# Optimization experiments

Hardware: AMD Instinct MI355X
Metric: run time of the kernel (lower is better)

The kernel has to match this reference:

```python
import jax, jax.numpy as jnp
import numpy as np

DIM = 384
HD = 64
SCALE = float(HD ** 0.5)


def _linear_params(key, out_f, in_f):
    kw, kb = jax.random.split(key)
    bound = 1.0 / np.sqrt(in_f)
    W = jax.random.uniform(kw, (out_f, in_f), jnp.float32, -bound, bound)
    b = jax.random.uniform(kb, (out_f,), jnp.float32, -bound, bound)
    return W, b


def setup_inputs() -> dict:
    key = jax.random.key(0)
    ks = jax.random.split(key, 12)
    N = 8192
    situation = jax.random.normal(ks[0], (DIM,), jnp.float32)
    turn_embeddings = jax.random.normal(ks[1], (N, DIM), jnp.float32)
    bilinear_scores = jax.random.normal(ks[2], (N,), jnp.float32)
    Wt, bt = _linear_params(ks[3], HD, DIM + 1)      # turn_proj
    Ws, bs = _linear_params(ks[4], HD, DIM)          # situation_proj
    Wsaq, bsaq = _linear_params(ks[5], HD, HD)
    Wsak, bsak = _linear_params(ks[6], HD, HD)
    Wsav, bsav = _linear_params(ks[7], HD, HD)
    Wcq, bcq = _linear_params(ks[8], HD, HD)
    Wck, bck = _linear_params(ks[9], HD, HD)
    Wcv, bcv = _linear_params(ks[10], HD, HD)
    # score_head is zero-initialized in the module; use small random values so
    # the output is non-trivial for kernel correctness testing.
    Wsc, bsc = _linear_params(ks[11], 1, HD)
    residual_gate = jnp.float32(-5.0)
    return dict(situation=situation, turn_embeddings=turn_embeddings,
                bilinear_scores=bilinear_scores,
                Wt=Wt, bt=bt, Ws=Ws, bs=bs,
                Wsaq=Wsaq, bsaq=bsaq, Wsak=Wsak, bsak=bsak, Wsav=Wsav, bsav=bsav,
                Wcq=Wcq, bcq=bcq, Wck=Wck, bck=bck, Wcv=Wcv, bcv=bcv,
                Wsc=Wsc, bsc=bsc, residual_gate=residual_gate)


def reference(situation, turn_embeddings, bilinear_scores,
              Wt, bt, Ws, bs,
              Wsaq, bsaq, Wsak, bsak, Wsav, bsav,
              Wcq, bcq, Wck, bck, Wcv, bcv,
              Wsc, bsc, residual_gate):
    # [N, dim+1] = [turn_embedding; bilinear_score]
    turn_features = jnp.concatenate([turn_embeddings, bilinear_scores[:, None]], axis=-1)
    turn_hidden = turn_features @ Wt.T + bt                      # [N, HD]
    # self-attention among turns (dropout = identity, eval mode)
    sa_q = turn_hidden @ Wsaq.T + bsaq
    sa_k = turn_hidden @ Wsak.T + bsak
    sa_v = turn_hidden @ Wsav.T + bsav
    sa_weights = jax.nn.softmax((sa_q @ sa_k.T) / SCALE, axis=-1)  # [N, N]
    turn_hidden = turn_hidden + sa_weights @ sa_v
    # sigmoid cross-attention against the single situation vector
    sit_hidden = (situation @ Ws.T + bs)[None, :]                # [1, HD]
    ca_q = turn_hidden @ Wcq.T + bcq                             # [N, HD]
    ca_k = sit_hidden @ Wck.T + bck                              # [1, HD]
    ca_v = sit_hidden @ Wcv.T + bcv                              # [1, HD]
    ca_weights = jax.nn.sigmoid((ca_q @ ca_k.T) / SCALE)         # [N, 1]
    combined = turn_hidden + ca_weights * ca_v                   # [N, HD]
    attention_scores = (combined @ Wsc.T + bsc)[:, 0]            # [N]
    gate = jax.nn.sigmoid(residual_gate)
    return (1.0 - gate) * bilinear_scores + gate * attention_scores
```

## Files before the change

kernel.cpp:

```cpp
#include <hip/hip_runtime.h>
#include <hip/hip_bf16.h>

typedef __attribute__((ext_vector_type(8))) short short8;
typedef __attribute__((ext_vector_type(4))) float f32x4;
typedef __attribute__((ext_vector_type(2))) long long2t;

__device__ __forceinline__ short f2bf(float x) {
  union { float f; unsigned u; } a; a.f = x;
  unsigned r = (a.u + 0x7FFFu + ((a.u >> 16) & 1u)) >> 16;
  return (short)r;
}
__device__ __forceinline__ float bf2f(short x) {
  union { unsigned u; float f; } a; a.u = ((unsigned)(unsigned short)x) << 16;
  return a.f;
}
__device__ __forceinline__ unsigned cvtpk(float lo, float hi) {
  unsigned r;
  asm("v_cvt_pk_bf16_f32 %0, %1, %2" : "=v"(r) : "v"(lo), "v"(hi));
  return r;
}
__device__ __forceinline__ unsigned pk8(float a, float b, float c, float d) {
  unsigned lo, hi;
  asm("v_cvt_pk_fp8_f32 %0, %1, %2" : "=v"(lo) : "v"(a), "v"(b));
  asm("v_cvt_pk_fp8_f32 %0, %1, %2" : "=v"(hi) : "v"(c), "v"(d));
  return (lo & 0xffffu) | (hi << 16);
}
__device__ __forceinline__ long2t as_l2(uint4 v) {
  union { uint4 u; long2t l; } cc; cc.u = v; return cc.l;
}
__device__ __forceinline__ void gload16(const void* g, void* l) {
  __builtin_amdgcn_global_load_lds((const __attribute__((address_space(1))) unsigned int*)g,
                                   (__attribute__((address_space(3))) unsigned int*)l, 16, 0, 0);
}

__global__ __launch_bounds__(256) void ca_proj4(
    const float* __restrict__ te, const float* __restrict__ bil,
    const float* __restrict__ Wt, const float* __restrict__ bt,
    const float* __restrict__ Wsaq, const float* __restrict__ bq,
    const float* __restrict__ Wsak, const float* __restrict__ bk2,
    const float* __restrict__ Wsav, const float* __restrict__ bv,
    short* __restrict__ hb, unsigned char* __restrict__ qb8,
    unsigned char* __restrict__ kb8, unsigned char* __restrict__ vl8,
    const float* __restrict__ sit, const float* __restrict__ Ws, const float* __restrict__ bs,
    const float* __restrict__ Wck, const float* __restrict__ bck,
    const float* __restrict__ Wcv, const float* __restrict__ bcv,
    const float* __restrict__ Wcq, const float* __restrict__ bcq,
    const float* __restrict__ Wsc, float* __restrict__ u_ws, float* __restrict__ scal,
    int N) {
  __shared__ float Pp[8192];
  __shared__ short Hl[32][72];
  __shared__ unsigned char Q8[32][72];
  __shared__ unsigned char K8[32][72];
  __shared__ unsigned char V8s[64][32];
  __shared__ float part[4][64];
  __shared__ float sh[64], ck[64], cv[64];
  const int t = threadIdx.x;
  if ((int)blockIdx.x == (N >> 5)) {
    int j = t & 63, p = t >> 6;
    float a = 0.f;
    for (int d = p * 96; d < p * 96 + 96; ++d) a += Ws[j * 384 + d] * sit[d];
    part[p][j] = a;
    __syncthreads();
    if (t < 64) sh[t] = part[0][t] + part[1][t] + part[2][t] + part[3][t] + bs[t];
    __syncthreads();
    if (t < 64) {
      float kk = bck[t], vv = bcv[t];
      for (int d = 0; d < 64; ++d) { kk += Wck[t * 64 + d] * sh[d]; vv += Wcv[t * 64 + d] * sh[d]; }
      ck[t] = kk; cv[t] = vv;
    }
    __syncthreads();
    if (t < 64) {
      float uu = 0.f;
      for (int jj = 0; jj < 64; ++jj) uu += Wcq[jj * 64 + t] * ck[jj];
      u_ws[t] = uu;
    }
    if (t == 0) {
      float c0 = 0.f, cw = 0.f;
      for (int jj = 0; jj < 64; ++jj) { c0 += bcq[jj] * ck[jj]; cw += cv[jj] * Wsc[jj]; }
      scal[0] = c0; scal[1] = cw;
    }
    return;
  }
  const int lane = t & 63, w = t >> 6;
  const int g = lane >> 4, li = lane & 15;
  const int i0 = blockIdx.x * 32;

  f32x4 acc[2][4];
#pragma unroll
  for (int qs = 0; qs < 2; ++qs)
#pragma unroll
    for (int n = 0; n < 4; ++n) acc[qs][n] = (f32x4){0.f, 0.f, 0.f, 0.f};
  const int kw = w * 96;
#pragma unroll
  for (int ks = 0; ks < 3; ++ks) {
    short8 af[2];
#pragma unroll
    for (int qs = 0; qs < 2; ++qs) {
      const float* ap = te + (size_t)(i0 + qs * 16 + li) * 384 + kw + ks * 32 + g * 8;
      float4 a0 = *(const float4*)ap;
      float4 a1 = *(const float4*)(ap + 4);
      af[qs][0] = f2bf(a0.x); af[qs][1] = f2bf(a0.y); af[qs][2] = f2bf(a0.z); af[qs][3] = f2bf(a0.w);
      af[qs][4] = f2bf(a1.x); af[qs][5] = f2bf(a1.y); af[qs][6] = f2bf(a1.z); af[qs][7] = f2bf(a1.w);
    }
#pragma unroll
    for (int n = 0; n < 4; ++n) {
      short8 bf;
      const float* wp = Wt + (size_t)(n * 16 + li) * 385 + kw + ks * 32 + g * 8;
#pragma unroll
      for (int jj = 0; jj < 8; ++jj) bf[jj] = f2bf(wp[jj]);
      acc[0][n] = __builtin_amdgcn_mfma_f32_16x16x32_bf16(af[0], bf, acc[0][n], 0, 0, 0);
      acc[1][n] = __builtin_amdgcn_mfma_f32_16x16x32_bf16(af[1], bf, acc[1][n], 0, 0, 0);
    }
  }
#pragma unroll
  for (int qs = 0; qs < 2; ++qs)
#pragma unroll
    for (int n = 0; n < 4; ++n)
      *(f32x4*)&Pp[((w * 8 + qs * 4 + n) * 64 + lane) * 4] = acc[qs][n];
  __syncthreads();
#pragma unroll
  for (int ss = 0; ss < 2; ++ss) {
    int s = t + ss * 256;
    int qs2 = s >> 8, n2 = (s >> 6) & 3, lane2 = s & 63;
    int g2 = lane2 >> 4, li2 = lane2 & 15;
    int base = (qs2 * 4 + n2) * 256 + lane2 * 4;
    f32x4 v0 = *(const f32x4*)&Pp[base];
    f32x4 v1 = *(const f32x4*)&Pp[base + 2048];
    f32x4 v2 = *(const f32x4*)&Pp[base + 4096];
    f32x4 v3 = *(const f32x4*)&Pp[base + 6144];
    int col = n2 * 16 + li2;
    float wc = Wt[(size_t)col * 385 + 384], bb = bt[col];
#pragma unroll
    for (int r = 0; r < 4; ++r) {
      int row = qs2 * 16 + g2 * 4 + r;
      float val = v0[r] + v1[r] + v2[r] + v3[r] + bb + bil[i0 + row] * wc;
      Hl[row][col] = f2bf(val);
    }
  }
  __syncthreads();
  {
    int row = t >> 3, seg = t & 7;
    *(uint4*)&hb[(size_t)(i0 + row) * 64 + seg * 8] = *(uint4*)&Hl[row][seg * 8];
  }
  short8 ha[2][2];
#pragma unroll
  for (int qs = 0; qs < 2; ++qs)
#pragma unroll
    for (int ks = 0; ks < 2; ++ks)
      ha[qs][ks] = *(const short8*)&Hl[qs * 16 + li][ks * 32 + g * 8];
  const float* Wm[3] = {Wsaq, Wsak, Wsav};
  f32x4 pacc[3][2];
#pragma unroll
  for (int m = 0; m < 3; ++m)
#pragma unroll
    for (int qs = 0; qs < 2; ++qs) pacc[m][qs] = (f32x4){0.f, 0.f, 0.f, 0.f};
#pragma unroll
  for (int m = 0; m < 3; ++m)
#pragma unroll
    for (int ks = 0; ks < 2; ++ks) {
      const float* wp = Wm[m] + (size_t)(w * 16 + li) * 64 + ks * 32 + g * 8;
      float4 b0 = *(const float4*)wp;
      float4 b1 = *(const float4*)(wp + 4);
      short8 bf;
      bf[0] = f2bf(b0.x); bf[1] = f2bf(b0.y); bf[2] = f2bf(b0.z); bf[3] = f2bf(b0.w);
      bf[4] = f2bf(b1.x); bf[5] = f2bf(b1.y); bf[6] = f2bf(b1.z); bf[7] = f2bf(b1.w);
      pacc[m][0] = __builtin_amdgcn_mfma_f32_16x16x32_bf16(ha[0][ks], bf, pacc[m][0], 0, 0, 0);
      pacc[m][1] = __builtin_amdgcn_mfma_f32_16x16x32_bf16(ha[1][ks], bf, pacc[m][1], 0, 0, 0);
    }
  const int col = w * 16 + li;
  const float QSC = 0.18033688011112042f;
  {
    float bbq = bq[col], bbk = bk2[col], bbv = bv[col];
#pragma unroll
    for (int qs = 0; qs < 2; ++qs) {
      unsigned uq = pk8((pacc[0][qs][0] + bbq) * QSC, (pacc[0][qs][1] + bbq) * QSC,
                        (pacc[0][qs][2] + bbq) * QSC, (pacc[0][qs][3] + bbq) * QSC);
      unsigned uk = pk8(pacc[1][qs][0] + bbk, pacc[1][qs][1] + bbk,
                        pacc[1][qs][2] + bbk, pacc[1][qs][3] + bbk);
      unsigned uv = pk8(pacc[2][qs][0] + bbv, pacc[2][qs][1] + bbv,
                        pacc[2][qs][2] + bbv, pacc[2][qs][3] + bbv);
#pragma unroll
      for (int r = 0; r < 4; ++r) {
        Q8[qs * 16 + g * 4 + r][col] = (unsigned char)(uq >> (8 * r));
        K8[qs * 16 + g * 4 + r][col] = (unsigned char)(uk >> (8 * r));
      }
      *(unsigned*)&V8s[col][qs * 16 + g * 4] = uv;
    }
  }
  __syncthreads();
  {
    const int h = t & 1, l2 = (t >> 1) & 63, loc = t >> 7;
    const int srow = (l2 & 15) + 16 * loc;
    const int scol = h * 32 + (l2 >> 4) * 8;
    unsigned long vq = *(const unsigned long*)&Q8[srow][scol];
    *(unsigned long*)(qb8 + ((size_t)((i0 >> 4) + loc) * 1024 + l2 * 16 + h * 8)) = vq;
    unsigned long vk = *(const unsigned long*)&K8[srow][scol];
    *(unsigned long*)(kb8 + ((size_t)((i0 >> 6) * 4 + ((i0 >> 4) & 3) + loc) * 1024 + l2 * 16 + h * 8)) = vk;
    const int dt = t >> 6, l3 = t & 63;
    unsigned long vv = *(const unsigned long*)&V8s[dt * 16 + (l3 & 15)][(l3 >> 4) * 8];
    *(unsigned long*)(vl8 + ((size_t)((i0 >> 6) * 4 + dt) * 1024 + l3 * 16 + ((i0 >> 5) & 1) * 8)) = vv;
  }
}

__global__ __launch_bounds__(128, 2) void ca_attn7(
    const uint4* __restrict__ qb8, const unsigned* __restrict__ kb8,
    const unsigned* __restrict__ vl8,
    unsigned* __restrict__ pOu, float* __restrict__ pL, int N) {
  __shared__ unsigned Kl[2][1024];
  __shared__ unsigned Vl[2][1024];
  __shared__ unsigned Pl[2][2][256];
  const int t = threadIdx.x, lane = t & 63, wid = t >> 6;
  const int g = lane >> 4, li = lane & 15;
  const int bid = blockIdx.x;
  const int sp = bid & 7, qblk = bid >> 3;
  const int i0 = qblk * 64 + wid * 32;
  const int ntil = N >> 9;
  const int tile0 = sp * ntil;

#define STG(b, T)                                                                                  \
  do {                                                                                             \
    gload16(kb8 + (((size_t)(T) * 4 + 2 * wid) << 8) + lane * 4,     &Kl[b][(2 * wid) * 256]);     \
    gload16(kb8 + (((size_t)(T) * 4 + 2 * wid + 1) << 8) + lane * 4, &Kl[b][(2 * wid + 1) * 256]); \
    gload16(vl8 + (((size_t)(T) * 4 + 2 * wid) << 8) + lane * 4,     &Vl[b][(2 * wid) * 256]);     \
    gload16(vl8 + (((size_t)(T) * 4 + 2 * wid + 1) << 8) + lane * 4, &Vl[b][(2 * wid + 1) * 256]); \
  } while (0)

  long2t qf[2];
  qf[0] = as_l2(qb8[(size_t)((i0 >> 4) + 0) * 64 + lane]);
  qf[1] = as_l2(qb8[(size_t)((i0 >> 4) + 1) * 64 + lane]);

  f32x4 acc[2][4];
  float rs[2] = {0.f, 0.f};
#pragma unroll
  for (int qs = 0; qs < 2; ++qs)
#pragma unroll
    for (int n = 0; n < 4; ++n) acc[qs][n] = (f32x4){0.f, 0.f, 0.f, 0.f};

  STG(0, tile0);
  asm volatile("s_waitcnt vmcnt(0)" ::: "memory");

  for (int tt = 0; tt < ntil; ++tt) {
    const int cur = tt & 1;
    __builtin_amdgcn_s_barrier();
    if (tt + 1 < ntil) STG(cur ^ 1, tile0 + tt + 1);

    f32x4 s4[2][4];
#pragma unroll
    for (int qs = 0; qs < 2; ++qs)
#pragma unroll
      for (int t4 = 0; t4 < 4; ++t4) s4[qs][t4] = (f32x4){0.f, 0.f, 0.f, 0.f};
    __builtin_amdgcn_s_setprio(1);
#pragma unroll
    for (int t4 = 0; t4 < 4; ++t4) {
      long2t kl = as_l2(*(const uint4*)&Kl[cur][t4 * 256 + lane * 4]);
      s4[0][t4] = __builtin_amdgcn_mfma_f32_16x16x32_fp8_fp8(kl.x, qf[0].x, s4[0][t4], 0, 0, 0);
      s4[0][t4] = __builtin_amdgcn_mfma_f32_16x16x32_fp8_fp8(kl.y, qf[0].y, s4[0][t4], 0, 0, 0);
      s4[1][t4] = __builtin_amdgcn_mfma_f32_16x16x32_fp8_fp8(kl.x, qf[1].x, s4[1][t4], 0, 0, 0);
      s4[1][t4] = __builtin_amdgcn_mfma_f32_16x16x32_fp8_fp8(kl.y, qf[1].y, s4[1][t4], 0, 0, 0);
    }
    __builtin_amdgcn_s_setprio(0);
#pragma unroll
    for (int qs = 0; qs < 2; ++qs) {
#pragma unroll
      for (int t4 = 0; t4 < 4; ++t4) {
        float p0, p1, p2, p3;
        asm("v_exp_f32 %0, %1" : "=v"(p0) : "v"(s4[qs][t4][0]));
        asm("v_exp_f32 %0, %1" : "=v"(p1) : "v"(s4[qs][t4][1]));
        asm("v_exp_f32 %0, %1" : "=v"(p2) : "v"(s4[qs][t4][2]));
        asm("v_exp_f32 %0, %1" : "=v"(p3) : "v"(s4[qs][t4][3]));
        rs[qs] += (p0 + p1) + (p2 + p3);
        unsigned u = pk8(p0, p1, p2, p3);
        Pl[wid][qs][(li + 16 * ((t4 & 1) * 2 + (g >> 1))) * 4 + (t4 >> 1) * 2 + (g & 1)] = u;
      }
    }
    asm volatile("s_waitcnt lgkmcnt(0)" ::: "memory");
    long2t pf0 = as_l2(*(const uint4*)&Pl[wid][0][lane * 4]);
    long2t pf1 = as_l2(*(const uint4*)&Pl[wid][1][lane * 4]);
    __builtin_amdgcn_s_setprio(1);
#pragma unroll
    for (int dt = 0; dt < 4; ++dt) {
      long2t vf = as_l2(*(const uint4*)&Vl[cur][dt * 256 + lane * 4]);
      acc[0][dt] = __builtin_amdgcn_mfma_f32_16x16x32_fp8_fp8(pf0.x, vf.x, acc[0][dt], 0, 0, 0);
      acc[0][dt] = __builtin_amdgcn_mfma_f32_16x16x32_fp8_fp8(pf0.y, vf.y, acc[0][dt], 0, 0, 0);
      acc[1][dt] = __builtin_amdgcn_mfma_f32_16x16x32_fp8_fp8(pf1.x, vf.x, acc[1][dt], 0, 0, 0);
      acc[1][dt] = __builtin_amdgcn_mfma_f32_16x16x32_fp8_fp8(pf1.y, vf.y, acc[1][dt], 0, 0, 0);
    }
    __builtin_amdgcn_s_setprio(0);
    asm volatile("s_waitcnt vmcnt(0)" ::: "memory");
  }
#undef STG

  const size_t ob = ((size_t)sp * (N >> 5) + (i0 >> 5)) * 2;
#pragma unroll
  for (int qs = 0; qs < 2; ++qs) {
#pragma unroll
    for (int dt = 0; dt < 4; ++dt) {
      uint2 wv;
      wv.x = cvtpk(acc[qs][dt][0], acc[qs][dt][1]);
      wv.y = cvtpk(acc[qs][dt][2], acc[qs][dt][3]);
      *(uint2*)&pOu[((ob + qs) * 4 + dt) * 128 + lane * 2] = wv;
    }
    float r2 = rs[qs] + __shfl_xor(rs[qs], 16, 64);
    r2 += __shfl_xor(r2, 32, 64);
    if (lane < 16) pL[(size_t)sp * N + i0 + qs * 16 + lane] = r2;
  }
}

__global__ __launch_bounds__(256) void ca_merge3(
    const short* __restrict__ hb, const unsigned* __restrict__ pOu, const float* __restrict__ pL,
    const float* __restrict__ u_ws, const float* __restrict__ scal,
    const float* __restrict__ bil, const float* __restrict__ Wsc,
    const float* __restrict__ bsc_p, const float* __restrict__ rgate_p,
    float* __restrict__ out, int N) {
  const int t = threadIdx.x;
  const int rp = t >> 3, e = t & 7;
  const int dt2 = e >> 1, li0 = (e & 1) * 8;
  const float gate = 1.f / (1.f + __expf(-rgate_p[0]));
  const float bsc = bsc_p[0], sc0 = scal[0], sc1 = scal[1];
  const int R0 = blockIdx.x * 64 + rp * 2;
  const int b32 = R0 >> 5, qs2 = (R0 >> 4) & 1, g2 = (R0 >> 2) & 3;
  const int rpair = (R0 & 3) >> 1;
  float o0[8], o1[8], L0 = 0.f, L1 = 0.f;
#pragma unroll
  for (int j = 0; j < 8; ++j) { o0[j] = 0.f; o1[j] = 0.f; }
#pragma unroll
  for (int sp2 = 0; sp2 < 8; ++sp2) {
    size_t base = ((((size_t)sp2 * (N >> 5) + b32) * 2 + qs2) * 4 + dt2) * 128
                  + (g2 * 16 + li0) * 2 + rpair;
#pragma unroll
    for (int j = 0; j < 8; ++j) {
      unsigned u = pOu[base + 2 * j];
      o0[j] += bf2f((short)(u & 0xffff));
      o1[j] += bf2f((short)(u >> 16));
    }
    L0 += pL[(size_t)sp2 * N + R0];
    L1 += pL[(size_t)sp2 * N + R0 + 1];
  }
  const float iL0 = 1.f / L0, iL1 = 1.f / L1;
  const int c0 = dt2 * 16 + li0;
  short8 hv0 = *(const short8*)&hb[(size_t)R0 * 64 + c0];
  short8 hv1 = *(const short8*)&hb[(size_t)(R0 + 1) * 64 + c0];
  float s1a = 0.f, s2a = 0.f, s1b = 0.f, s2b = 0.f;
#pragma unroll
  for (int j = 0; j < 8; ++j) {
    float uwsj = u_ws[c0 + j], wscj = Wsc[c0 + j];
    float h0 = bf2f(hv0[j]) + o0[j] * iL0;
    float h1 = bf2f(hv1[j]) + o1[j] * iL1;
    s1a += h0 * uwsj; s2a += h0 * wscj;
    s1b += h1 * uwsj; s2b += h1 * wscj;
  }
#pragma unroll
  for (int mask = 1; mask < 8; mask <<= 1) {
    s1a += __shfl_xor(s1a, mask, 64);
    s2a += __shfl_xor(s2a, mask, 64);
    s1b += __shfl_xor(s1b, mask, 64);
    s2b += __shfl_xor(s2b, mask, 64);
  }
  if (e == 0) {
    float cawa = 1.f / (1.f + __expf(-(s1a + sc0) * 0.125f));
    float cawb = 1.f / (1.f + __expf(-(s1b + sc0) * 0.125f));
    float scoreA = s2a + cawa * sc1 + bsc;
    float scoreB = s2b + cawb * sc1 + bsc;
    out[R0] = (1.f - gate) * bil[R0] + gate * scoreA;
    out[R0 + 1] = (1.f - gate) * bil[R0 + 1] + gate * scoreB;
  }
}

extern "C" void kernel_launch(void* const* d_in, const int* in_sizes, int n_in,
                              void* d_out, int out_size, void* d_ws, size_t ws_size,
                              hipStream_t stream) {
  const float* sit  = (const float*)d_in[0];
  const float* te   = (const float*)d_in[1];
  const float* bil  = (const float*)d_in[2];
  const float* Wt   = (const float*)d_in[3];
  const float* bt   = (const float*)d_in[4];
  const float* Ws   = (const float*)d_in[5];
  const float* bs   = (const float*)d_in[6];
  const float* Wsaq = (const float*)d_in[7];
  const float* bsaq = (const float*)d_in[8];
  const float* Wsak = (const float*)d_in[9];
  const float* bsak = (const float*)d_in[10];
  const float* Wsav = (const float*)d_in[11];
  const float* bsav = (const float*)d_in[12];
  const float* Wcq  = (const float*)d_in[13];
  const float* bcq  = (const float*)d_in[14];
  const float* Wck  = (const float*)d_in[15];
  const float* bck  = (const float*)d_in[16];
  const float* Wcv  = (const float*)d_in[17];
  const float* bcv  = (const float*)d_in[18];
  const float* Wsc  = (const float*)d_in[19];
  const float* bsc  = (const float*)d_in[20];
  const float* rgate= (const float*)d_in[21];
  const int N = in_sizes[2];

  char* w = (char*)d_ws;
  size_t off = 0;
  short* hbuf        = (short*)(w + off);         off += (size_t)N * 64 * 2;
  unsigned char* qb8 = (unsigned char*)(w + off); off += (size_t)N * 64;
  unsigned char* kb8 = (unsigned char*)(w + off); off += (size_t)N * 64;
  unsigned char* vl8 = (unsigned char*)(w + off); off += (size_t)N * 64;
  float* u_ws        = (float*)(w + off);         off += 64 * 4;
  float* scal        = (float*)(w + off);         off += 4 * 4;
  unsigned* pOu      = (unsigned*)(w + off);      off += (size_t)8 * N * 64 * 2;
  float* pL          = (float*)(w + off);         off += (size_t)8 * N * 4;

  ca_proj4<<<N / 32 + 1, 256, 0, stream>>>(te, bil, Wt, bt, Wsaq, bsaq, Wsak, bsak,
                                           Wsav, bsav, hbuf, qb8, kb8, vl8,
                                           sit, Ws, bs, Wck, bck, Wcv, bcv, Wcq, bcq, Wsc,
                                           u_ws, scal, N);
  ca_attn7<<<N / 8, 128, 0, stream>>>((const uint4*)qb8, (const unsigned*)kb8,
                                      (const unsigned*)vl8, pOu, pL, N);
  ca_merge3<<<N / 64, 256, 0, stream>>>(hbuf, pOu, pL, u_ws, scal, bil, Wsc, bsc, rgate,
                                        (float*)d_out, N);
}
```

Measured before the change: 50.56 us.

## Split turn projection by output columns per wave, drop split-K LDS reduction

The first projection GEMM changes from a split-K layout (each wave covering a quarter of K for all 64 output columns, then reducing partial sums through a 32KB shared buffer) to an output-column split where each wave owns 16 columns across the full K. This removes the partial-sum LDS buffer, one barrier and the reduction pass, and lowers LDS use, which may allow more blocks per CU. In exchange every wave now reads the whole 32x384 activation tile from global memory, four times the previous per-wave A traffic, and runs a longer serial chain of dependent MFMAs.

```diff
diff --git a/kernel.cpp b/kernel.cpp
--- a/kernel.cpp
+++ b/kernel.cpp
@@ -33,7 +33,7 @@
                                    (__attribute__((address_space(3))) unsigned int*)l, 16, 0, 0);
 }
 
-__global__ __launch_bounds__(256) void ca_proj4(
+__global__ __launch_bounds__(256) void ca_proj6(
     const float* __restrict__ te, const float* __restrict__ bil,
     const float* __restrict__ Wt, const float* __restrict__ bt,
     const float* __restrict__ Wsaq, const float* __restrict__ bq,
@@ -47,7 +47,6 @@
     const float* __restrict__ Wcq, const float* __restrict__ bcq,
     const float* __restrict__ Wsc, float* __restrict__ u_ws, float* __restrict__ scal,
     int N) {
-  __shared__ float Pp[8192];
   __shared__ short Hl[32][72];
   __shared__ unsigned char Q8[32][72];
   __shared__ unsigned char K8[32][72];
@@ -84,58 +83,39 @@
   const int lane = t & 63, w = t >> 6;
   const int g = lane >> 4, li = lane & 15;
   const int i0 = blockIdx.x * 32;
-
-  f32x4 acc[2][4];
-#pragma unroll
-  for (int qs = 0; qs < 2; ++qs)
-#pragma unroll
-    for (int n = 0; n < 4; ++n) acc[qs][n] = (f32x4){0.f, 0.f, 0.f, 0.f};
-  const int kw = w * 96;
-#pragma unroll
-  for (int ks = 0; ks < 3; ++ks) {
+  const int col = w * 16 + li;
+
+  f32x4 acc[2];
+  acc[0] = (f32x4){0.f, 0.f, 0.f, 0.f};
+  acc[1] = (f32x4){0.f, 0.f, 0.f, 0.f};
+  const float* wrow = Wt + (size_t)col * 385 + g * 8;
+#pragma unroll 3
+  for (int ks = 0; ks < 12; ++ks) {
     short8 af[2];
 #pragma unroll
     for (int qs = 0; qs < 2; ++qs) {
-      const float* ap = te + (size_t)(i0 + qs * 16 + li) * 384 + kw + ks * 32 + g * 8;
+      const float* ap = te + (size_t)(i0 + qs * 16 + li) * 384 + ks * 32 + g * 8;
       float4 a0 = *(const float4*)ap;
       float4 a1 = *(const float4*)(ap + 4);
       af[qs][0] = f2bf(a0.x); af[qs][1] = f2bf(a0.y); af[qs][2] = f2bf(a0.z); af[qs][3] = f2bf(a0.w);
       af[qs][4] = f2bf(a1.x); af[qs][5] = f2bf(a1.y); af[qs][6] = f2bf(a1.z); af[qs][7] = f2bf(a1.w);
     }
-#pragma unroll
-    for (int n = 0; n < 4; ++n) {
-      short8 bf;
-      const float* wp = Wt + (size_t)(n * 16 + li) * 385 + kw + ks * 32 + g * 8;
-#pragma unroll
-      for (int jj = 0; jj < 8; ++jj) bf[jj] = f2bf(wp[jj]);
-      acc[0][n] = __builtin_amdgcn_mfma_f32_16x16x32_bf16(af[0], bf, acc[0][n], 0, 0, 0);
-      acc[1][n] = __builtin_amdgcn_mfma_f32_16x16x32_bf16(af[1], bf, acc[1][n], 0, 0, 0);
-    }
-  }
-#pragma unroll
-  for (int qs = 0; qs < 2; ++qs)
-#pragma unroll
-    for (int n = 0; n < 4; ++n)
-      *(f32x4*)&Pp[((w * 8 + qs * 4 + n) * 64 + lane) * 4] = acc[qs][n];
-  __syncthreads();
-#pragma unroll
-  for (int ss = 0; ss < 2; ++ss) {
-    int s = t + ss * 256;
-    int qs2 = s >> 8, n2 = (s >> 6) & 3, lane2 = s & 63;
-    int g2 = lane2 >> 4, li2 = lane2 & 15;
-    int base = (qs2 * 4 + n2) * 256 + lane2 * 4;
-    f32x4 v0 = *(const f32x4*)&Pp[base];
-    f32x4 v1 = *(const f32x4*)&Pp[base + 2048];
-    f32x4 v2 = *(const f32x4*)&Pp[base + 4096];
-    f32x4 v3 = *(const f32x4*)&Pp[base + 6144];
-    int col = n2 * 16 + li2;
-    float wc = Wt[(size_t)col * 385 + 384], bb = bt[col];
-#pragma unroll
-    for (int r = 0; r < 4; ++r) {
-      int row = qs2 * 16 + g2 * 4 + r;
-      float val = v0[r] + v1[r] + v2[r] + v3[r] + bb + bil[i0 + row] * wc;
-      Hl[row][col] = f2bf(val);
-    }
+    short8 bf;
+    const float* wp = wrow + ks * 32;
+#pragma unroll
+    for (int jj = 0; jj < 8; ++jj) bf[jj] = f2bf(wp[jj]);
+    acc[0] = __builtin_amdgcn_mfma_f32_16x16x32_bf16(af[0], bf, acc[0], 0, 0, 0);
+    acc[1] = __builtin_amdgcn_mfma_f32_16x16x32_bf16(af[1], bf, acc[1], 0, 0, 0);
+  }
+  {
+    const float bb = bt[col], wc = Wt[(size_t)col * 385 + 384];
+#pragma unroll
+    for (int qs = 0; qs < 2; ++qs)
+#pragma unroll
+      for (int r = 0; r < 4; ++r) {
+        int row = qs * 16 + g * 4 + r;
+        Hl[row][col] = f2bf(acc[qs][r] + bb + bil[i0 + row] * wc);
+      }
   }
   __syncthreads();
   {
@@ -158,7 +138,7 @@
   for (int m = 0; m < 3; ++m)
 #pragma unroll
     for (int ks = 0; ks < 2; ++ks) {
-      const float* wp = Wm[m] + (size_t)(w * 16 + li) * 64 + ks * 32 + g * 8;
+      const float* wp = Wm[m] + (size_t)col * 64 + ks * 32 + g * 8;
       float4 b0 = *(const float4*)wp;
       float4 b1 = *(const float4*)(wp + 4);
       short8 bf;
@@ -167,7 +147,6 @@
       pacc[m][0] = __builtin_amdgcn_mfma_f32_16x16x32_bf16(ha[0][ks], bf, pacc[m][0], 0, 0, 0);
       pacc[m][1] = __builtin_amdgcn_mfma_f32_16x16x32_bf16(ha[1][ks], bf, pacc[m][1], 0, 0, 0);
     }
-  const int col = w * 16 + li;
   const float QSC = 0.18033688011112042f;
   {
     float bbq = bq[col], bbk = bk2[col], bbv = bv[col];
@@ -404,7 +383,7 @@
   unsigned* pOu      = (unsigned*)(w + off);      off += (size_t)8 * N * 64 * 2;
   float* pL          = (float*)(w + off);         off += (size_t)8 * N * 4;
 
-  ca_proj4<<<N / 32 + 1, 256, 0, stream>>>(te, bil, Wt, bt, Wsaq, bsaq, Wsak, bsak,
+  ca_proj6<<<N / 32 + 1, 256, 0, stream>>>(te, bil, Wt, bt, Wsaq, bsaq, Wsak, bsak,
                                            Wsav, bsav, hbuf, qb8, kb8, vl8,
                                            sit, Ws, bs, Wck, bck, Wcv, bcv, Wcq, bcq, Wsc,
                                            u_ws, scal, N);
```

Result: slower. 53.66 us (+6.1%).

## Split attention keys 16 ways and store partial outputs as fp8

Applied to the files above, without the earlier changes.

Doubles the key-split factor in the attention kernel from 8 to 16, launching twice as many blocks with a higher occupancy hint. Partial output accumulators are packed to fp8 instead of bf16, so each split's partial-output buffer is half the size. The merge kernel decodes them with a software fp8 decoder and sums 16 splits. This aims to add parallelism and cut partial-output traffic, but it costs merge work, pL traffic and accuracy, since unnormalized partial sums are quantized to fp8 (range/precision risk).

```diff
diff --git a/kernel.cpp b/kernel.cpp
--- a/kernel.cpp
+++ b/kernel.cpp
@@ -24,6 +24,12 @@
   asm("v_cvt_pk_fp8_f32 %0, %1, %2" : "=v"(lo) : "v"(a), "v"(b));
   asm("v_cvt_pk_fp8_f32 %0, %1, %2" : "=v"(hi) : "v"(c), "v"(d));
   return (lo & 0xffffu) | (hi << 16);
+}
+__device__ __forceinline__ float fp8d(unsigned b) {
+  int e = (b >> 3) & 15, m = b & 7;
+  int K = e ? ((8 + m) << (e - 1)) : m;
+  float v = (float)K * 0.001953125f;
+  return (b & 0x80) ? -v : v;
 }
 __device__ __forceinline__ long2t as_l2(uint4 v) {
   union { uint4 u; long2t l; } cc; cc.u = v; return cc.l;
@@ -202,7 +208,7 @@
   }
 }
 
-__global__ __launch_bounds__(128, 2) void ca_attn7(
+__global__ __launch_bounds__(128, 4) void ca_attn8(
     const uint4* __restrict__ qb8, const unsigned* __restrict__ kb8,
     const unsigned* __restrict__ vl8,
     unsigned* __restrict__ pOu, float* __restrict__ pL, int N) {
@@ -212,9 +218,9 @@
   const int t = threadIdx.x, lane = t & 63, wid = t >> 6;
   const int g = lane >> 4, li = lane & 15;
   const int bid = blockIdx.x;
-  const int sp = bid & 7, qblk = bid >> 3;
+  const int sp = bid & 15, qblk = bid >> 4;
   const int i0 = qblk * 64 + wid * 32;
-  const int ntil = N >> 9;
+  const int ntil = N >> 10;
   const int tile0 = sp * ntil;
 
 #define STG(b, T)                                                                                  \
@@ -295,10 +301,8 @@
   for (int qs = 0; qs < 2; ++qs) {
 #pragma unroll
     for (int dt = 0; dt < 4; ++dt) {
-      uint2 wv;
-      wv.x = cvtpk(acc[qs][dt][0], acc[qs][dt][1]);
-      wv.y = cvtpk(acc[qs][dt][2], acc[qs][dt][3]);
-      *(uint2*)&pOu[((ob + qs) * 4 + dt) * 128 + lane * 2] = wv;
+      unsigned u = pk8(acc[qs][dt][0], acc[qs][dt][1], acc[qs][dt][2], acc[qs][dt][3]);
+      pOu[((ob + qs) * 4 + dt) * 64 + lane] = u;
     }
     float r2 = rs[qs] + __shfl_xor(rs[qs], 16, 64);
     r2 += __shfl_xor(r2, 32, 64);
@@ -306,7 +310,7 @@
   }
 }
 
-__global__ __launch_bounds__(256) void ca_merge3(
+__global__ __launch_bounds__(256) void ca_merge4(
     const short* __restrict__ hb, const unsigned* __restrict__ pOu, const float* __restrict__ pL,
     const float* __restrict__ u_ws, const float* __restrict__ scal,
     const float* __restrict__ bil, const float* __restrict__ Wsc,
@@ -319,19 +323,19 @@
   const float bsc = bsc_p[0], sc0 = scal[0], sc1 = scal[1];
   const int R0 = blockIdx.x * 64 + rp * 2;
   const int b32 = R0 >> 5, qs2 = (R0 >> 4) & 1, g2 = (R0 >> 2) & 3;
-  const int rpair = (R0 & 3) >> 1;
+  const int r0 = R0 & 3;
   float o0[8], o1[8], L0 = 0.f, L1 = 0.f;
 #pragma unroll
   for (int j = 0; j < 8; ++j) { o0[j] = 0.f; o1[j] = 0.f; }
 #pragma unroll
-  for (int sp2 = 0; sp2 < 8; ++sp2) {
-    size_t base = ((((size_t)sp2 * (N >> 5) + b32) * 2 + qs2) * 4 + dt2) * 128
-                  + (g2 * 16 + li0) * 2 + rpair;
+  for (int sp2 = 0; sp2 < 16; ++sp2) {
+    size_t base = ((((size_t)sp2 * (N >> 5) + b32) * 2 + qs2) * 4 + dt2) * 64
+                  + g2 * 16 + li0;
 #pragma unroll
     for (int j = 0; j < 8; ++j) {
-      unsigned u = pOu[base + 2 * j];
-      o0[j] += bf2f((short)(u & 0xffff));
-      o1[j] += bf2f((short)(u >> 16));
+      unsigned u = pOu[base + j];
+      o0[j] += fp8d((u >> (8 * r0)) & 0xff);
+      o1[j] += fp8d((u >> (8 * (r0 + 1))) & 0xff);
     }
     L0 += pL[(size_t)sp2 * N + R0];
     L1 += pL[(size_t)sp2 * N + R0 + 1];
@@ -401,15 +405,15 @@
   unsigned char* vl8 = (unsigned char*)(w + off); off += (size_t)N * 64;
   float* u_ws        = (float*)(w + off);         off += 64 * 4;
   float* scal        = (float*)(w + off);         off += 4 * 4;
-  unsigned* pOu      = (unsigned*)(w + off);      off += (size_t)8 * N * 64 * 2;
-  float* pL          = (float*)(w + off);         off += (size_t)8 * N * 4;
+  unsigned* pOu      = (unsigned*)(w + off);      off += (size_t)16 * N * 16 * 4;
+  float* pL          = (float*)(w + off);         off += (size_t)16 * N * 4;
 
   ca_proj4<<<N / 32 + 1, 256, 0, stream>>>(te, bil, Wt, bt, Wsaq, bsaq, Wsak, bsak,
                                            Wsav, bsav, hbuf, qb8, kb8, vl8,
                                            sit, Ws, bs, Wck, bck, Wcv, bcv, Wcq, bcq, Wsc,
                                            u_ws, scal, N);
-  ca_attn7<<<N / 8, 128, 0, stream>>>((const uint4*)qb8, (const unsigned*)kb8,
+  ca_attn8<<<N / 4, 128, 0, stream>>>((const uint4*)qb8, (const unsigned*)kb8,
                                       (const unsigned*)vl8, pOu, pL, N);
-  ca_merge3<<<N / 64, 256, 0, stream>>>(hbuf, pOu, pL, u_ws, scal, bil, Wsc, bsc, rgate,
+  ca_merge4<<<N / 64, 256, 0, stream>>>(hbuf, pOu, pL, u_ws, scal, bil, Wsc, bsc, rgate,
                                         (float*)d_out, N);
 }
```

New measurement: 52.78 us. +4.4%, slower.
